# Optimization experiments

Measured on AMD Instinct MI355X. Metric: run time of the kernel, lower is better.

Reference implementation:

```python
import jax, jax.numpy as jnp
import numpy as np

B, L, PD, DIM, H, DH, DEPTH, MLP, NIMG, NCLS, TH = 2, 2048, 768, 512, 8, 64, 2, 2048, 4, 1000, 32


def _ln(x, g):
    # bias-free LayerNorm (beta buffer is zeros), eps matches torch F.layer_norm
    mu = jnp.mean(x, axis=-1, keepdims=True)
    var = jnp.var(x, axis=-1, keepdims=True)
    return (x - mu) / jnp.sqrt(var + 1e-5) * g


def _rms(x, g):
    # F.normalize(dim=-1) * sqrt(dim_head) * gamma; x: [b,h,n,dh], g: [h,1,dh]
    n = jnp.linalg.norm(x, axis=-1, keepdims=True)
    return x / jnp.maximum(n, 1e-12) * (DH ** 0.5) * g


def _attn(x, context, mask, ln_g, qg, kg, Wq, Wkv, Wo):
    b, n = x.shape[0], x.shape[1]
    xn = _ln(x, ln_g)
    kv = xn if context is None else context  # context is NOT pre-normed (matches source)
    m = kv.shape[1]
    q = (xn @ Wq).reshape(b, n, H, DH).transpose(0, 2, 1, 3)   # [b,h,n,dh]
    k, v = jnp.split(kv @ Wkv, 2, axis=-1)
    k = k.reshape(b, m, H, DH).transpose(0, 2, 1, 3)
    v = v.reshape(b, m, H, DH).transpose(0, 2, 1, 3)
    q = _rms(q, qg)
    k = _rms(k, kg)
    dots = jnp.einsum('bhid,bhjd->bhij', q, k)  # no 1/sqrt(d): QK-RMSNorm carries the scale
    neg = -jnp.finfo(dots.dtype).max
    dots = jnp.where(mask, dots, neg)
    a = jax.nn.softmax(dots, axis=-1)
    out = jnp.einsum('bhij,bhjd->bhid', a, v)
    out = out.transpose(0, 2, 1, 3).reshape(b, n, H * DH)
    return out @ Wo


def _forward(patches, ln_pe1_g, W_pe, b_pe, ln_pe2_g, pos_h_emb, pos_w_emb,
             attn_ln_g, q_g, k_g, Wq, Wkv, Wo, ff_ln_g, W1, b1, W2, b2,
             final_ln_g, pool_q, pool_ln_g, pool_q_g, pool_k_g,
             pool_Wq, pool_Wkv, pool_Wo, head_ln_g, W_head,
             pos_h, pos_w, image_ids):
    # patch embedding: LN -> Linear -> LN, then factorized 2D pos embed
    x = _ln(patches, ln_pe1_g) @ W_pe + b_pe
    x = _ln(x, ln_pe2_g)
    x = x + pos_h_emb[pos_h] + pos_w_emb[pos_w]
    # block-diagonal attention mask: tokens attend only within their image
    mask = (image_ids[:, None, :, None] == image_ids[:, None, None, :])  # [B,1,L,L]
    for i in range(DEPTH):
        x = _attn(x, None, mask, attn_ln_g[i], q_g[i], k_g[i], Wq[i], Wkv[i], Wo[i]) + x
        h = _ln(x, ff_ln_g[i]) @ W1[i] + b1[i]
        h = jax.nn.gelu(h, approximate=False)
        x = h @ W2[i] + b2[i] + x
    x = _ln(x, final_ln_g)
    # attention pooling: one learned query per packed image
    queries = jnp.broadcast_to(pool_q, (B, NIMG, DIM))
    pmask = (jnp.arange(NIMG)[None, None, :, None] == image_ids[:, None, None, :])  # [B,1,NIMG,L]
    pooled = _attn(queries, x, pmask, pool_ln_g, pool_q_g, pool_k_g, pool_Wq, pool_Wkv, pool_Wo) + queries
    return _ln(pooled, head_ln_g) @ W_head  # [B, NIMG, NCLS]


def setup_inputs() -> dict:
    key = jax.random.key(0)
    ks = jax.random.split(key, 16)
    s = 0.02
    inp = {}
    inp['patches'] = jax.random.normal(ks[0], (B, L, PD), jnp.float32)
    inp['pos_h'] = jax.random.randint(ks[1], (B, L), 0, TH)
    inp['pos_w'] = jax.random.randint(ks[2], (B, L), 0, TH)
    inp['image_ids'] = jnp.sort(jax.random.randint(ks[3], (B, L), 0, NIMG), axis=-1)
    inp['ln_pe1_g'] = jnp.ones((PD,), jnp.float32)
    inp['W_pe'] = jax.random.normal(ks[4], (PD, DIM), jnp.float32) * s
    inp['b_pe'] = jnp.zeros((DIM,), jnp.float32)
    inp['ln_pe2_g'] = jnp.ones((DIM,), jnp.float32)
    inp['pos_h_emb'] = jax.random.normal(ks[5], (TH, DIM), jnp.float32)
    inp['pos_w_emb'] = jax.random.normal(ks[6], (TH, DIM), jnp.float32)
    inp['attn_ln_g'] = jnp.ones((DEPTH, DIM), jnp.float32)
    inp['q_g'] = jnp.ones((DEPTH, H, 1, DH), jnp.float32)
    inp['k_g'] = jnp.ones((DEPTH, H, 1, DH), jnp.float32)
    inp['Wq'] = jax.random.normal(ks[7], (DEPTH, DIM, H * DH), jnp.float32) * s
    inp['Wkv'] = jax.random.normal(ks[8], (DEPTH, DIM, 2 * H * DH), jnp.float32) * s
    inp['Wo'] = jax.random.normal(ks[9], (DEPTH, H * DH, DIM), jnp.float32) * s
    inp['ff_ln_g'] = jnp.ones((DEPTH, DIM), jnp.float32)
    inp['W1'] = jax.random.normal(ks[10], (DEPTH, DIM, MLP), jnp.float32) * s
    inp['b1'] = jnp.zeros((DEPTH, MLP), jnp.float32)
    inp['W2'] = jax.random.normal(ks[11], (DEPTH, MLP, DIM), jnp.float32) * s
    inp['b2'] = jnp.zeros((DEPTH, DIM), jnp.float32)
    inp['final_ln_g'] = jnp.ones((DIM,), jnp.float32)
    inp['pool_q'] = jax.random.normal(ks[12], (DIM,), jnp.float32)
    inp['pool_ln_g'] = jnp.ones((DIM,), jnp.float32)
    inp['pool_q_g'] = jnp.ones((H, 1, DH), jnp.float32)
    inp['pool_k_g'] = jnp.ones((H, 1, DH), jnp.float32)
    inp['pool_Wq'] = jax.random.normal(ks[13], (DIM, H * DH), jnp.float32) * s
    inp['pool_Wkv'] = jax.random.normal(ks[14], (DIM, 2 * H * DH), jnp.float32) * s
    inp['pool_Wo'] = jax.random.normal(ks[15], (H * DH, DIM), jnp.float32) * s
    inp['head_ln_g'] = jnp.ones((DIM,), jnp.float32)
    inp['W_head'] = jax.random.normal(jax.random.fold_in(key, 99), (DIM, NCLS), jnp.float32) * s
    return inp


def reference(patches, pos_h, pos_w, image_ids, ln_pe1_g, W_pe, b_pe, ln_pe2_g,
              pos_h_emb, pos_w_emb, attn_ln_g, q_g, k_g, Wq, Wkv, Wo, ff_ln_g,
              W1, b1, W2, b2, final_ln_g, pool_q, pool_ln_g, pool_q_g, pool_k_g,
              pool_Wq, pool_Wkv, pool_Wo, head_ln_g, W_head):
    return _forward(patches, ln_pe1_g, W_pe, b_pe, ln_pe2_g, pos_h_emb, pos_w_emb,
                    attn_ln_g, q_g, k_g, Wq, Wkv, Wo, ff_ln_g, W1, b1, W2, b2,
                    final_ln_g, pool_q, pool_ln_g, pool_q_g, pool_k_g,
                    pool_Wq, pool_Wkv, pool_Wo, head_ln_g, W_head,
                    pos_h, pos_w, image_ids)
```

## Files before the change

### kernel.cpp

```cpp
#include <hip/hip_runtime.h>
#include <hip/hip_bf16.h>
#include <cfloat>
#include <math.h>

#define BB 2
#define LL 2048
#define PD 768
#define DIM 512
#define HH 8
#define DH 64
#define DEPTH 2
#define MLP 2048
#define NIMG 4
#define NCLS 1000
#define ROWS (BB*LL)
#define QKV (3*DIM)
#define NEGBIG (-1e30f)

typedef __hip_bfloat16 bf16;
typedef __bf16 v8bf __attribute__((ext_vector_type(8)));
typedef float f32x4 __attribute__((ext_vector_type(4)));

__device__ __forceinline__ float ldin(const void* p, size_t i, int bf) {
    return bf ? __bfloat162float(((const bf16*)p)[i]) : ((const float*)p)[i];
}
__device__ __forceinline__ float lda(const float* p, size_t i) { return p[i]; }
__device__ __forceinline__ float lda(const bf16* p, size_t i) { return __bfloat162float(p[i]); }
__device__ __forceinline__ void st(float* p, size_t i, float v) { p[i] = v; }
__device__ __forceinline__ void st(bf16* p, size_t i, float v) { p[i] = __float2bfloat16(v); }
__device__ __forceinline__ unsigned short f2bf(float x) {
    return __builtin_bit_cast(unsigned short, __float2bfloat16(x));
}
__device__ __forceinline__ float us2f(unsigned short u) {
    return __bfloat162float(__builtin_bit_cast(bf16, u));
}

__device__ __forceinline__ void stage16(const void* gsrc, void* ldst)
{
    __builtin_amdgcn_global_load_lds(
        (const __attribute__((address_space(1))) unsigned int*)(unsigned long long)gsrc,
        (__attribute__((address_space(3))) unsigned int*)(unsigned int)(unsigned long long)ldst,
        16, 0, 0);
}

__global__ void detect_dtype_kernel(const void* ones, int* flag)
{
    if (threadIdx.x == 0 && blockIdx.x == 0)
        *flag = (((const unsigned*)ones)[0] == 0x3F803F80u) ? 1 : 0;
}

__global__ void wconv_kernel(const void* __restrict__ W, int K, int N, size_t inStride,
                             bf16* __restrict__ out, size_t outOff, size_t outStride,
                             const int* dtf)
{
    __shared__ float t[32][33];
    const int bf = *dtf;
    const size_t zin = (size_t)blockIdx.z * inStride;
    const size_t zout = outOff + (size_t)blockIdx.z * outStride;
    const int kb = blockIdx.y * 32, nb = blockIdx.x * 32;
    const int tx = threadIdx.x, ty = threadIdx.y;
    #pragma unroll
    for (int u = 0; u < 4; ++u)
        t[ty + 8 * u][tx] = ldin(W, zin + (size_t)(kb + ty + 8 * u) * N + nb + tx, bf);
    __syncthreads();
    #pragma unroll
    for (int u = 0; u < 4; ++u)
        out[zout + (size_t)(nb + ty + 8 * u) * K + kb + tx] = __float2bfloat16(t[tx][ty + 8 * u]);
}

template<int RAWIN, typename TOUT>
__global__ void ln_kernel(const void* __restrict__ in, const void* __restrict__ g, size_t goff,
                          TOUT* __restrict__ out, int D, const int* dtf)
{
    __shared__ float red[16];
    const int bf = *dtf;
    const int row = blockIdx.x, tid = threadIdx.x;
    const size_t base = (size_t)row * D;
    float s = 0.f, ss = 0.f;
    for (int d = tid; d < D; d += blockDim.x) {
        float v = RAWIN ? ldin(in, base + d, bf) : ((const float*)in)[base + d];
        s += v; ss += v * v;
    }
    for (int o = 32; o; o >>= 1) { s += __shfl_xor(s, o); ss += __shfl_xor(ss, o); }
    const int wid = tid >> 6, lane = tid & 63, nw = blockDim.x >> 6;
    if (lane == 0) { red[wid] = s; red[8 + wid] = ss; }
    __syncthreads();
    if (tid == 0) {
        float a = 0.f, b = 0.f;
        for (int w = 0; w < nw; ++w) { a += red[w]; b += red[8 + w]; }
        red[0] = a; red[8] = b;
    }
    __syncthreads();
    const float mean = red[0] / D;
    const float var  = red[8] / D - mean * mean;
    const float rstd = rsqrtf(var + 1e-5f);
    for (int d = tid; d < D; d += blockDim.x) {
        float v = RAWIN ? ldin(in, base + d, bf) : ((const float*)in)[base + d];
        st(out, base + d, (v - mean) * rstd * ldin(g, goff + d, bf));
    }
}

__global__ void ln_pos_kernel(float* __restrict__ x, const void* __restrict__ g,
                              const void* __restrict__ phe, const void* __restrict__ pwe,
                              const int* __restrict__ ph, const int* __restrict__ pw,
                              const int* dtf)
{
    __shared__ float red[16];
    const int bf = *dtf;
    const int row = blockIdx.x, tid = threadIdx.x;
    const size_t base = (size_t)row * DIM;
    float s = 0.f, ss = 0.f;
    for (int d = tid; d < DIM; d += 256) { float v = x[base + d]; s += v; ss += v * v; }
    for (int o = 32; o; o >>= 1) { s += __shfl_xor(s, o); ss += __shfl_xor(ss, o); }
    const int wid = tid >> 6, lane = tid & 63;
    if (lane == 0) { red[wid] = s; red[8 + wid] = ss; }
    __syncthreads();
    if (tid == 0) {
        float a = 0.f, b = 0.f;
        for (int w = 0; w < 4; ++w) { a += red[w]; b += red[8 + w]; }
        red[0] = a; red[8] = b;
    }
    __syncthreads();
    const float mean = red[0] / DIM;
    const float var  = red[8] / DIM - mean * mean;
    const float rstd = rsqrtf(var + 1e-5f);
    const size_t hoff = (size_t)ph[row] * DIM, woff = (size_t)pw[row] * DIM;
    for (int d = tid; d < DIM; d += 256) {
        float v = (x[base + d] - mean) * rstd * ldin(g, d, bf)
                + ldin(phe, hoff + d, bf) + ldin(pwe, woff + d, bf);
        x[base + d] = v;
    }
}

#define GM 128
#define GN 64
#define GK 64

template<typename TO, int EPI>
__global__ void mgemm_kernel(const bf16* __restrict__ A, const bf16* __restrict__ Wt,
                             const void* __restrict__ bias, size_t boff,
                             const float* __restrict__ resid, TO* __restrict__ out,
                             int M, int N, int K, int kc, int gelu, const int* dtf)
{
    __shared__ __align__(16) unsigned short As[GM][GK];
    __shared__ __align__(16) unsigned short Bs[GN][GK];
    const int tid = threadIdx.x;
    const int w = tid >> 6, l = tid & 63, g = l >> 4, c = l & 15;
    const int wm = (w >> 1) * 64, wn = (w & 1) * 32;
    const int m0 = blockIdx.y * GM, n0 = blockIdx.x * GN;
    const int kbeg = blockIdx.z * kc, kend = kbeg + kc;
    const int lrow = l >> 3, lcol = (l & 7) * 8;

    f32x4 acc[4][2] = {};

    for (int k0 = kbeg; k0 < kend; k0 += GK) {
        __syncthreads();
        #pragma unroll
        for (int u = 0; u < 4; ++u) {
            const int rr = 32 * w + 8 * u;
            stage16(A + (size_t)(m0 + rr + lrow) * K + k0 + lcol, &As[rr][0]);
        }
        #pragma unroll
        for (int u = 0; u < 2; ++u) {
            const int rr = 16 * w + 8 * u;
            stage16(Wt + (size_t)(n0 + rr + lrow) * K + k0 + lcol, &Bs[rr][0]);
        }
        __syncthreads();
        #pragma unroll
        for (int kk = 0; kk < GK; kk += 32) {
            v8bf av[4], bv[2];
            #pragma unroll
            for (int i = 0; i < 4; ++i) av[i] = *(const v8bf*)&As[wm + i * 16 + c][kk + 8 * g];
            #pragma unroll
            for (int j = 0; j < 2; ++j) bv[j] = *(const v8bf*)&Bs[wn + j * 16 + c][kk + 8 * g];
            #pragma unroll
            for (int i = 0; i < 4; ++i)
                #pragma unroll
                for (int j = 0; j < 2; ++j)
                    acc[i][j] = __builtin_amdgcn_mfma_f32_16x16x32_bf16(av[i], bv[j], acc[i][j], 0, 0, 0);
        }
    }

    if (EPI == 0) {
        float* po = (float*)out + (size_t)blockIdx.z * M * N;
        #pragma unroll
        for (int i = 0; i < 4; ++i) {
            const int rb = m0 + wm + i * 16 + 4 * g;
            #pragma unroll
            for (int j = 0; j < 2; ++j) {
                const int col = n0 + wn + j * 16 + c;
                #pragma unroll
                for (int r = 0; r < 4; ++r)
                    po[(size_t)(rb + r) * N + col] = acc[i][j][r];
            }
        }
    } else {
        const int bf = *dtf;
        #pragma unroll
        for (int i = 0; i < 4; ++i) {
            const int rb = m0 + wm + i * 16 + 4 * g;
            #pragma unroll
            for (int j = 0; j < 2; ++j) {
                const int col = n0 + wn + j * 16 + c;
                const float bvl = bias ? ldin(bias, boff + col, bf) : 0.f;
                #pragma unroll
                for (int r = 0; r < 4; ++r) {
                    float v = acc[i][j][r] + bvl;
                    if (gelu) v = 0.5f * v * (1.f + erff(v * 0.70710678118654752f));
                    if (resid) v += resid[(size_t)(rb + r) * N + col];
                    st(out, (size_t)(rb + r) * N + col, v);
                }
            }
        }
    }
}

template<typename TO>
__global__ void mcomb_kernel(const float* __restrict__ part, int S, const void* __restrict__ bias,
                             size_t boff, const float* __restrict__ resid, TO* __restrict__ out,
                             size_t MN, int N, int gelu, const int* dtf)
{
    const size_t idx = (size_t)blockIdx.x * 256 + threadIdx.x;
    if (idx >= MN) return;
    float v = 0.f;
    for (int s = 0; s < S; ++s) v += part[(size_t)s * MN + idx];
    const int bf = *dtf;
    if (bias) v += ldin(bias, boff + (int)(idx % N), bf);
    if (gelu) v = 0.5f * v * (1.f + erff(v * 0.70710678118654752f));
    if (resid) v += resid[idx];
    st(out, idx, v);
}

__global__ void comb_ln_kernel(const float* __restrict__ part, int S,
                               const void* __restrict__ bias, size_t boff,
                               float* __restrict__ x, const void* __restrict__ g, size_t goff,
                               bf16* __restrict__ xb, const int* dtf)
{
    __shared__ float red[16];
    const int bf = *dtf;
    const int row = blockIdx.x, tid = threadIdx.x;
    const size_t base = (size_t)row * DIM;
    float v[2];
    float s = 0.f, ss = 0.f;
    #pragma unroll
    for (int u = 0; u < 2; ++u) {
        const int d = tid + 256 * u;
        float a = 0.f;
        for (int sc = 0; sc < S; ++sc) a += part[(size_t)sc * ROWS * DIM + base + d];
        if (bias) a += ldin(bias, boff + d, bf);
        a += x[base + d];
        x[base + d] = a;
        v[u] = a; s += a; ss += a * a;
    }
    for (int o = 32; o; o >>= 1) { s += __shfl_xor(s, o); ss += __shfl_xor(ss, o); }
    const int wid = tid >> 6, lane = tid & 63;
    if (lane == 0) { red[wid] = s; red[8 + wid] = ss; }
    __syncthreads();
    if (tid == 0) {
        float a = 0.f, b = 0.f;
        for (int w2 = 0; w2 < 4; ++w2) { a += red[w2]; b += red[8 + w2]; }
        red[0] = a; red[8] = b;
    }
    __syncthreads();
    const float mean = red[0] / DIM;
    const float var  = red[8] / DIM - mean * mean;
    const float rstd = rsqrtf(var + 1e-5f);
    #pragma unroll
    for (int u = 0; u < 2; ++u) {
        const int d = tid + 256 * u;
        xb[base + d] = __float2bfloat16((v[u] - mean) * rstd * ldin(g, goff + d, bf));
    }
}

#define TS 16
template<typename TA, typename TO>
__global__ void gemm_kernel(const TA* __restrict__ A, const void* __restrict__ W, size_t woff,
                            const void* __restrict__ bias, size_t boff,
                            const float* __restrict__ resid, TO* __restrict__ out,
                            int M, int N, int K, int gelu, const int* dtf)
{
    __shared__ float As[TS][TS + 1];
    __shared__ float Bs[TS][TS + 1];
    const int bf = *dtf;
    const int tx = threadIdx.x, ty = threadIdx.y;
    const int col = blockIdx.x * TS + tx;
    const int row = blockIdx.y * TS + ty;
    float acc = 0.f;
    for (int k0 = 0; k0 < K; k0 += TS) {
        const int ka = k0 + tx;
        As[ty][tx] = (row < M && ka < K) ? lda(A, (size_t)row * K + ka) : 0.f;
        const int kb = k0 + ty;
        Bs[ty][tx] = (col < N && kb < K) ? ldin(W, woff + (size_t)kb * N + col, bf) : 0.f;
        __syncthreads();
        #pragma unroll
        for (int kk = 0; kk < TS; ++kk) acc = fmaf(As[ty][kk], Bs[kk][tx], acc);
        __syncthreads();
    }
    if (row < M && col < N) {
        if (bias) acc += ldin(bias, boff + col, bf);
        if (gelu) acc = 0.5f * acc * (1.f + erff(acc * 0.70710678118654752f));
        if (resid) acc += resid[(size_t)row * N + col];
        st(out, (size_t)row * N + col, acc);
    }
}

__global__ void rms_kernel(float* __restrict__ buf, const void* __restrict__ g, size_t goff,
                           int stride, int colbase, const int* dtf)
{
    const int bf = *dtf;
    const int r = blockIdx.x, h = blockIdx.y, lane = threadIdx.x;
    float* p = buf + (size_t)r * stride + colbase + h * DH;
    const float v = p[lane];
    float ss = v * v;
    for (int o = 32; o; o >>= 1) ss += __shfl_xor(ss, o);
    const float norm = sqrtf(ss);
    const float sc = 8.0f / fmaxf(norm, 1e-12f);
    p[lane] = v * sc * ldin(g, goff + h * DH + lane, bf);
}

__global__ void rms2_kernel(bf16* __restrict__ buf, int stride,
                            const void* __restrict__ g0, size_t g0off,
                            int base1, const void* __restrict__ g1, size_t g1off,
                            int nslot, const int* dtf)
{
    const int bf = *dtf;
    const int tid = threadIdx.x;
    const int s = tid >> 4, li = tid & 15;
    if (s >= nslot) return;
    const int h = s & 7;
    const int colbase = (s < 8) ? 0 : base1;
    const void* g = (s < 8) ? g0 : g1;
    const size_t go = ((s < 8) ? g0off : g1off) + h * DH + li * 4;
    bf16* p = buf + (size_t)blockIdx.x * stride + colbase + h * DH + li * 4;
    ushort4 v = *(const ushort4*)p;
    const float f0 = us2f(v.x), f1 = us2f(v.y), f2 = us2f(v.z), f3 = us2f(v.w);
    float ss = f0 * f0 + f1 * f1 + f2 * f2 + f3 * f3;
    ss += __shfl_xor(ss, 8); ss += __shfl_xor(ss, 4);
    ss += __shfl_xor(ss, 2); ss += __shfl_xor(ss, 1);
    const float sc = 8.0f / fmaxf(sqrtf(ss), 1e-12f);
    ushort4 o;
    o.x = f2bf(f0 * sc * ldin(g, go + 0, bf));
    o.y = f2bf(f1 * sc * ldin(g, go + 1, bf));
    o.z = f2bf(f2 * sc * ldin(g, go + 2, bf));
    o.w = f2bf(f3 * sc * ldin(g, go + 3, bf));
    *(ushort4*)p = o;
}

#define QT 64
#define KT 64
#define LP 72

__global__ void flash_attn_kernel(const bf16* __restrict__ q, int qstr,
                                  const bf16* __restrict__ kpt, const bf16* __restrict__ vpt,
                                  int kvstr, const int* __restrict__ ids,
                                  bf16* __restrict__ out)
{
    __shared__ __align__(16) unsigned short Qs[QT][LP];
    __shared__ __align__(16) unsigned short Ks[KT][LP];
    __shared__ __align__(16) unsigned short Vt[DH][LP];
    __shared__ __align__(16) unsigned short Ps[QT][LP];
    __shared__ __align__(16) int ids_s[KT];
    __shared__ __align__(16) int qids_s[QT];
    __shared__ int range_s[2];

    const int tid = threadIdx.x;
    const int bid = blockIdx.x;
    const int s0 = (bid & 7) * 64 + (bid >> 3);
    const int qb = (s0 & 31) * QT;
    const int h = (s0 >> 5) & 7;
    const int b = s0 >> 8;
    const int w = tid >> 6, l = tid & 63, g = l >> 4, c = l & 15;

    {
        const int r = tid >> 2, c0 = (tid & 3) << 4;
        const bf16* qp = q + (size_t)(b * LL + qb + r) * qstr + h * DH + c0;
        *(int4*)&Qs[r][c0]     = *(const int4*)qp;
        *(int4*)&Qs[r][c0 + 8] = *(const int4*)(qp + 8);
        if (tid < QT) qids_s[tid] = ids[b * LL + qb + tid];
    }
    if (tid == 0) {
        const int* bp = ids + b * LL;
        const int qlo = bp[qb], qhi = bp[qb + QT - 1];
        int lo = 0, hi = LL;
        while (lo < hi) { int mid = (lo + hi) >> 1; if (bp[mid] < qlo) lo = mid + 1; else hi = mid; }
        range_s[0] = lo;
        int lo2 = 0, hi2 = LL;
        while (lo2 < hi2) { int mid = (lo2 + hi2) >> 1; if (bp[mid] <= qhi) lo2 = mid + 1; else hi2 = mid; }
        range_s[1] = lo2;
    }
    __syncthreads();

    const int myid = qids_s[16 * w + c];
    const v8bf qf0 = *(const v8bf*)&Qs[16 * w + c][8 * g];
    const v8bf qf1 = *(const v8bf*)&Qs[16 * w + c][8 * g + 32];
    const int kb_start = (range_s[0] / KT) * KT;
    const int kb_end = range_s[1];

    f32x4 o[4];
    #pragma unroll
    for (int dt = 0; dt < 4; ++dt) o[dt] = (f32x4){0.f, 0.f, 0.f, 0.f};
    float mr = NEGBIG, lr = 0.f;

    for (int kb = kb_start; kb < kb_end; kb += KT) {
        __syncthreads();
        {
            const int r = tid >> 2, c0 = (tid & 3) << 4;
            const bf16* kp = kpt + (size_t)(b * LL + kb + r) * kvstr + h * DH + c0;
            *(int4*)&Ks[r][c0]     = *(const int4*)kp;
            *(int4*)&Ks[r][c0 + 8] = *(const int4*)(kp + 8);
        }
        {
            const int kp2 = (tid & 31) * 2, db = (tid >> 5) * 8;
            const bf16* v0p = vpt + (size_t)(b * LL + kb + kp2) * kvstr + h * DH + db;
            const bf16* v1p = v0p + kvstr;
            const ushort4 a0 = *(const ushort4*)v0p;
            const ushort4 a1 = *(const ushort4*)(v0p + 4);
            const ushort4 b0 = *(const ushort4*)v1p;
            const ushort4 b1 = *(const ushort4*)(v1p + 4);
            const unsigned short* ap0 = (const unsigned short*)&a0;
            const unsigned short* ap1 = (const unsigned short*)&a1;
            const unsigned short* bp0 = (const unsigned short*)&b0;
            const unsigned short* bp1 = (const unsigned short*)&b1;
            #pragma unroll
            for (int j = 0; j < 4; ++j) {
                *(unsigned int*)&Vt[db + j][kp2]     = (unsigned)ap0[j] | ((unsigned)bp0[j] << 16);
                *(unsigned int*)&Vt[db + 4 + j][kp2] = (unsigned)ap1[j] | ((unsigned)bp1[j] << 16);
            }
        }
        if (tid < KT) ids_s[tid] = ids[b * LL + kb + tid];
        __syncthreads();

        f32x4 stt[4];
        #pragma unroll
        for (int t = 0; t < 4; ++t) {
            stt[t] = (f32x4){0.f, 0.f, 0.f, 0.f};
            v8bf kf0 = *(const v8bf*)&Ks[16 * t + c][8 * g];
            v8bf kf1 = *(const v8bf*)&Ks[16 * t + c][8 * g + 32];
            stt[t] = __builtin_amdgcn_mfma_f32_16x16x32_bf16(kf0, qf0, stt[t], 0, 0, 0);
            stt[t] = __builtin_amdgcn_mfma_f32_16x16x32_bf16(kf1, qf1, stt[t], 0, 0, 0);
        }

        float sv[16]; int mk[16];
        float tmax = NEGBIG;
        #pragma unroll
        for (int t = 0; t < 4; ++t) {
            int4 iv = *(const int4*)&ids_s[16 * t + 4 * g];
            const int* ivp = (const int*)&iv;
            #pragma unroll
            for (int r = 0; r < 4; ++r) {
                float s = stt[t][r];
                int m = (ivp[r] == myid);
                sv[4 * t + r] = s; mk[4 * t + r] = m;
                if (m) tmax = fmaxf(tmax, s);
            }
        }
        tmax = fmaxf(tmax, __shfl_xor(tmax, 16));
        tmax = fmaxf(tmax, __shfl_xor(tmax, 32));
        const float mnew = fmaxf(mr, tmax);
        const float al = __expf(mr - mnew);
        float tsum = 0.f;
        #pragma unroll
        for (int t = 0; t < 4; ++t) {
            ushort4 pk;
            unsigned short* pp = (unsigned short*)&pk;
            #pragma unroll
            for (int r = 0; r < 4; ++r) {
                float p = mk[4 * t + r] ? __expf(sv[4 * t + r] - mnew) : 0.f;
                tsum += p;
                pp[r] = f2bf(p);
            }
            *(ushort4*)&Ps[16 * w + c][16 * t + 4 * g] = pk;
        }
        tsum += __shfl_xor(tsum, 16);
        tsum += __shfl_xor(tsum, 32);
        lr = lr * al + tsum;
        mr = mnew;

        const float a0 = __shfl(al, 4 * g + 0);
        const float a1 = __shfl(al, 4 * g + 1);
        const float a2 = __shfl(al, 4 * g + 2);
        const float a3 = __shfl(al, 4 * g + 3);
        #pragma unroll
        for (int dt = 0; dt < 4; ++dt) {
            o[dt][0] *= a0; o[dt][1] *= a1; o[dt][2] *= a2; o[dt][3] *= a3;
        }

        const v8bf pf0 = *(const v8bf*)&Ps[16 * w + c][8 * g];
        const v8bf pf1 = *(const v8bf*)&Ps[16 * w + c][8 * g + 32];
        #pragma unroll
        for (int dt = 0; dt < 4; ++dt) {
            v8bf vf0 = *(const v8bf*)&Vt[16 * dt + c][8 * g];
            v8bf vf1 = *(const v8bf*)&Vt[16 * dt + c][8 * g + 32];
            o[dt] = __builtin_amdgcn_mfma_f32_16x16x32_bf16(pf0, vf0, o[dt], 0, 0, 0);
            o[dt] = __builtin_amdgcn_mfma_f32_16x16x32_bf16(pf1, vf1, o[dt], 0, 0, 0);
        }
    }

    const float li0 = 1.f / __shfl(lr, 4 * g + 0);
    const float li1 = 1.f / __shfl(lr, 4 * g + 1);
    const float li2 = 1.f / __shfl(lr, 4 * g + 2);
    const float li3 = 1.f / __shfl(lr, 4 * g + 3);
    #pragma unroll
    for (int dt = 0; dt < 4; ++dt) {
        bf16* op = out + (size_t)(b * LL + qb + 16 * w) * DIM + h * DH + 16 * dt + c;
        op[(size_t)(4 * g + 0) * DIM] = __float2bfloat16(o[dt][0] * li0);
        op[(size_t)(4 * g + 1) * DIM] = __float2bfloat16(o[dt][1] * li1);
        op[(size_t)(4 * g + 2) * DIM] = __float2bfloat16(o[dt][2] * li2);
        op[(size_t)(4 * g + 3) * DIM] = __float2bfloat16(o[dt][3] * li3);
    }
}

#define PCH 16
#define PCK (LL / PCH)

__global__ void pool_attn_part_kernel(const float* __restrict__ q, const bf16* __restrict__ kv,
                                      int kvs, const int* __restrict__ ids,
                                      float* __restrict__ ppm, float* __restrict__ ppl,
                                      float* __restrict__ ppo)
{
    const int iq = blockIdx.x & (NIMG - 1), ch = blockIdx.x >> 2;
    const int h = blockIdx.y, b = blockIdx.z;
    const int tid = threadIdx.x;
    const int qrow = b * NIMG + iq;
    const int j0 = ch * PCK;
    __shared__ float qs[DH];
    __shared__ float s[PCK];

    qs[tid] = q[(size_t)qrow * DIM + h * DH + tid];
    __syncthreads();
    #pragma unroll
    for (int u = 0; u < 2; ++u) {
        const int j = j0 + tid + 64 * u;
        const bf16* kp = kv + (size_t)(b * LL + j) * kvs + h * DH;
        float d = 0.f;
        #pragma unroll
        for (int t = 0; t < DH; t += 8) {
            int4 kvv = *(const int4*)&kp[t];
            const unsigned short* uu = (const unsigned short*)&kvv;
            #pragma unroll
            for (int z = 0; z < 8; ++z) d = fmaf(qs[t + z], us2f(uu[z]), d);
        }
        s[tid + 64 * u] = (ids[b * LL + j] == iq) ? d : NEGBIG;
    }
    __syncthreads();
    float m = fmaxf(s[tid], s[tid + 64]);
    for (int o = 32; o; o >>= 1) m = fmaxf(m, __shfl_xor(m, o));
    const float p0 = __expf(s[tid] - m), p1 = __expf(s[tid + 64] - m);
    float ls = p0 + p1;
    for (int o = 32; o; o >>= 1) ls += __shfl_xor(ls, o);
    s[tid] = p0; s[tid + 64] = p1;
    __syncthreads();
    float acc = 0.f;
    for (int jj = 0; jj < PCK; ++jj)
        acc += s[jj] * __bfloat162float(kv[(size_t)(b * LL + j0 + jj) * kvs + DIM + h * DH + tid]);
    const int p = ((b * HH + h) * NIMG + iq) * PCH + ch;
    if (tid == 0) { ppm[p] = m; ppl[p] = ls; }
    ppo[(size_t)p * DH + tid] = acc;
}

__global__ void pool_attn_comb_kernel(const float* __restrict__ ppm, const float* __restrict__ ppl,
                                      const float* __restrict__ ppo, float* __restrict__ out)
{
    const int iq = blockIdx.x, h = blockIdx.y, b = blockIdx.z;
    const int d = threadIdx.x;
    const int pb = ((b * HH + h) * NIMG + iq) * PCH;
    float mstar = NEGBIG;
    #pragma unroll
    for (int ch = 0; ch < PCH; ++ch) mstar = fmaxf(mstar, ppm[pb + ch]);
    float lsum = 0.f, osum = 0.f;
    #pragma unroll
    for (int ch = 0; ch < PCH; ++ch) {
        const float w = __expf(ppm[pb + ch] - mstar);
        lsum += ppl[pb + ch] * w;
        osum += ppo[(size_t)(pb + ch) * DH + d] * w;
    }
    out[(size_t)(b * NIMG + iq) * DIM + h * DH + d] = osum / lsum;
}

__global__ void fill_q_kernel(float* __restrict__ queries, const void* __restrict__ pool_q,
                              const int* dtf)
{
    const int bf = *dtf;
    const int idx = blockIdx.x * blockDim.x + threadIdx.x;
    if (idx < BB * NIMG * DIM) queries[idx] = ldin(pool_q, idx % DIM, bf);
}

__global__ void write_out_kernel(const float* __restrict__ in, void* __restrict__ out, int n,
                                 const int* dtf)
{
    const int bf = *dtf;
    const int idx = blockIdx.x * blockDim.x + threadIdx.x;
    if (idx < n) {
        if (bf) ((bf16*)out)[idx] = __float2bfloat16(in[idx]);
        else    ((float*)out)[idx] = in[idx];
    }
}

extern "C" void kernel_launch(void* const* d_in, const int* in_sizes, int n_in,
                              void* d_out, int out_size, void* d_ws, size_t ws_size,
                              hipStream_t stream)
{
    const void* patches   = d_in[0];
    const int*  pos_h     = (const int*) d_in[1];
    const int*  pos_w     = (const int*) d_in[2];
    const int*  image_ids = (const int*) d_in[3];
    const void* ln_pe1_g  = d_in[4];
    const void* W_pe      = d_in[5];
    const void* b_pe      = d_in[6];
    const void* ln_pe2_g  = d_in[7];
    const void* pos_h_emb = d_in[8];
    const void* pos_w_emb = d_in[9];
    const void* attn_ln_g = d_in[10];
    const void* q_g       = d_in[11];
    const void* k_g       = d_in[12];
    const void* Wq        = d_in[13];
    const void* Wkv       = d_in[14];
    const void* Wo        = d_in[15];
    const void* ff_ln_g   = d_in[16];
    const void* W1        = d_in[17];
    const void* b1        = d_in[18];
    const void* W2        = d_in[19];
    const void* b2        = d_in[20];
    const void* final_ln_g= d_in[21];
    const void* pool_q    = d_in[22];
    const void* pool_ln_g = d_in[23];
    const void* pool_q_g  = d_in[24];
    const void* pool_k_g  = d_in[25];
    const void* pool_Wq   = d_in[26];
    const void* pool_Wkv  = d_in[27];
    const void* pool_Wo   = d_in[28];
    const void* head_ln_g = d_in[29];
    const void* W_head    = d_in[30];

    char* p = (char*)d_ws;
    int* flag = (int*)p;                         p += 256;
    float* x   = (float*)p;                      p += (size_t)ROWS * DIM * 4;
    bf16* xb   = (bf16*)p;                       p += (size_t)ROWS * PD * 2;
    bf16* qkvb = (bf16*)p;  bf16* hb = qkvb;     p += (size_t)ROWS * MLP * 2;
    bf16* wpeT  = (bf16*)p;                      p += (size_t)DIM * PD * 2;
    bf16* wqkvT = (bf16*)p;                      p += (size_t)DEPTH * QKV * DIM * 2;
    bf16* woT   = (bf16*)p;                      p += (size_t)DEPTH * DIM * DIM * 2;
    bf16* w1T   = (bf16*)p;                      p += (size_t)DEPTH * MLP * DIM * 2;
    bf16* w2T   = (bf16*)p;                      p += (size_t)DEPTH * DIM * MLP * 2;
    bf16* pkvT  = (bf16*)p;                      p += (size_t)2 * DIM * DIM * 2;
    float* queries = (float*)p;                  p += 4096 * 4;
    float* qp      = (float*)p;                  p += 4096 * 4;
    float* pattn   = (float*)p;                  p += 4096 * 4;
    float* pooled  = (float*)p;                  p += 4096 * 4;
    bf16*  pln     = (bf16*)p;                   p += 4096 * 2;
    float* hout    = (float*)p;                  p += 8192 * 4;
    float* ppm     = (float*)p;                  p += 1024 * 4;
    float* ppl     = (float*)p;                  p += 1024 * 4;
    float* ppo     = (float*)p;                  p += (size_t)1024 * DH * 4;
    float* part    = (float*)p;                  p += (size_t)4 * ROWS * DIM * 4;

    const dim3 blk256(256);
    const dim3 blkG(TS, TS);
    const dim3 blkT(32, 8);

    detect_dtype_kernel<<<1, 1, 0, stream>>>(ln_pe1_g, flag);

    wconv_kernel<<<dim3(DIM / 32, PD / 32, 1), blkT, 0, stream>>>(
        W_pe, PD, DIM, 0, wpeT, 0, 0, flag);
    wconv_kernel<<<dim3(DIM / 32, DIM / 32, DEPTH), blkT, 0, stream>>>(
        Wq, DIM, DIM, (size_t)DIM * DIM, wqkvT, 0, (size_t)QKV * DIM, flag);
    wconv_kernel<<<dim3(2 * DIM / 32, DIM / 32, DEPTH), blkT, 0, stream>>>(
        Wkv, DIM, 2 * DIM, (size_t)DIM * 2 * DIM, wqkvT, (size_t)DIM * DIM, (size_t)QKV * DIM, flag);
    wconv_kernel<<<dim3(DIM / 32, DIM / 32, DEPTH), blkT, 0, stream>>>(
        Wo, DIM, DIM, (size_t)DIM * DIM, woT, 0, (size_t)DIM * DIM, flag);
    wconv_kernel<<<dim3(MLP / 32, DIM / 32, DEPTH), blkT, 0, stream>>>(
        W1, DIM, MLP, (size_t)DIM * MLP, w1T, 0, (size_t)MLP * DIM, flag);
    wconv_kernel<<<dim3(DIM / 32, MLP / 32, DEPTH), blkT, 0, stream>>>(
        W2, MLP, DIM, (size_t)MLP * DIM, w2T, 0, (size_t)DIM * MLP, flag);
    wconv_kernel<<<dim3(2 * DIM / 32, DIM / 32, 1), blkT, 0, stream>>>(
        pool_Wkv, DIM, 2 * DIM, 0, pkvT, 0, 0, flag);

    ln_kernel<1, bf16><<<ROWS, blk256, 0, stream>>>(patches, ln_pe1_g, 0, xb, PD, flag);
    mgemm_kernel<float, 0><<<dim3(DIM / GN, ROWS / GM, 2), blk256, 0, stream>>>(
        xb, wpeT, nullptr, 0, nullptr, part, ROWS, DIM, PD, PD / 2, 0, flag);
    mcomb_kernel<float><<<(ROWS * DIM + 255) / 256, blk256, 0, stream>>>(
        part, 2, b_pe, 0, nullptr, x, (size_t)ROWS * DIM, DIM, 0, flag);
    ln_pos_kernel<<<ROWS, blk256, 0, stream>>>(x, ln_pe2_g, pos_h_emb, pos_w_emb, pos_h, pos_w, flag);
    ln_kernel<0, bf16><<<ROWS, blk256, 0, stream>>>(x, attn_ln_g, 0, xb, DIM, flag);

    for (int i = 0; i < DEPTH; ++i) {
        mgemm_kernel<bf16, 1><<<dim3(QKV / GN, ROWS / GM, 1), blk256, 0, stream>>>(
            xb, wqkvT + (size_t)i * QKV * DIM, nullptr, 0, nullptr, qkvb,
            ROWS, QKV, DIM, DIM, 0, flag);
        rms2_kernel<<<ROWS, blk256, 0, stream>>>(
            qkvb, QKV, q_g, (size_t)i * HH * DH, DIM, k_g, (size_t)i * HH * DH, 16, flag);
        flash_attn_kernel<<<dim3(512), blk256, 0, stream>>>(
            qkvb, QKV, qkvb + DIM, qkvb + 2 * DIM, QKV, image_ids, xb);
        mgemm_kernel<float, 0><<<dim3(DIM / GN, ROWS / GM, 2), blk256, 0, stream>>>(
            xb, woT + (size_t)i * DIM * DIM, nullptr, 0, nullptr, part,
            ROWS, DIM, DIM, DIM / 2, 0, flag);
        comb_ln_kernel<<<ROWS, blk256, 0, stream>>>(
            part, 2, nullptr, 0, x, ff_ln_g, (size_t)i * DIM, xb, flag);
        mgemm_kernel<bf16, 1><<<dim3(MLP / GN, ROWS / GM, 1), blk256, 0, stream>>>(
            xb, w1T + (size_t)i * MLP * DIM, b1, (size_t)i * MLP, nullptr, hb,
            ROWS, MLP, DIM, DIM, 1, flag);
        mgemm_kernel<float, 0><<<dim3(DIM / GN, ROWS / GM, 4), blk256, 0, stream>>>(
            hb, w2T + (size_t)i * DIM * MLP, nullptr, 0, nullptr, part,
            ROWS, DIM, MLP, MLP / 4, 0, flag);
        const void* gnext = (i + 1 < DEPTH) ? attn_ln_g : final_ln_g;
        const size_t gnoff = (i + 1 < DEPTH) ? (size_t)(i + 1) * DIM : 0;
        comb_ln_kernel<<<ROWS, blk256, 0, stream>>>(
            part, 4, b2, (size_t)i * DIM, x, gnext, gnoff, xb, flag);
    }

    fill_q_kernel<<<(BB * NIMG * DIM + 255) / 256, blk256, 0, stream>>>(queries, pool_q, flag);
    ln_kernel<0, bf16><<<BB * NIMG, blk256, 0, stream>>>(queries, pool_ln_g, 0, pln, DIM, flag);
    gemm_kernel<bf16, float><<<dim3(DIM / TS, 1), blkG, 0, stream>>>(
        pln, pool_Wq, 0, nullptr, 0, nullptr, qp, BB * NIMG, DIM, DIM, 0, flag);
    mgemm_kernel<bf16, 1><<<dim3(2 * DIM / GN, ROWS / GM, 1), blk256, 0, stream>>>(
        xb, pkvT, nullptr, 0, nullptr, qkvb, ROWS, 2 * DIM, DIM, DIM, 0, flag);
    rms_kernel<<<dim3(BB * NIMG, HH), dim3(64), 0, stream>>>(
        qp, pool_q_g, 0, DIM, 0, flag);
    rms2_kernel<<<ROWS, blk256, 0, stream>>>(
        qkvb, 2 * DIM, pool_k_g, 0, 0, nullptr, 0, 8, flag);
    pool_attn_part_kernel<<<dim3(NIMG * PCH, HH, BB), dim3(64), 0, stream>>>(
        qp, qkvb, 2 * DIM, image_ids, ppm, ppl, ppo);
    pool_attn_comb_kernel<<<dim3(NIMG, HH, BB), dim3(64), 0, stream>>>(ppm, ppl, ppo, pattn);
    gemm_kernel<float, float><<<dim3(DIM / TS, 1), blkG, 0, stream>>>(
        pattn, pool_Wo, 0, nullptr, 0, queries, pooled, BB * NIMG, DIM, DIM, 0, flag);

    ln_kernel<0, bf16><<<BB * NIMG, blk256, 0, stream>>>(pooled, head_ln_g, 0, pln, DIM, flag);
    gemm_kernel<bf16, float><<<dim3((NCLS + TS - 1) / TS, 1), blkG, 0, stream>>>(
        pln, W_head, 0, nullptr, 0, nullptr, hout, BB * NIMG, NCLS, DIM, 0, flag);
    write_out_kernel<<<(BB * NIMG * NCLS + 255) / 256, blk256, 0, stream>>>(
        hout, d_out, BB * NIMG * NCLS, flag);
}
```

Before: 473.4 us.

## Fuse patch-embed combine, LN and pos-embed; stream K from global in attention

Measured after the change: 495.4 us. 4.7% more time.

```diff
diff --git a/kernel.cpp b/kernel.cpp
--- a/kernel.cpp
+++ b/kernel.cpp
@@ -100,35 +100,69 @@
     }
 }
 
-__global__ void ln_pos_kernel(float* __restrict__ x, const void* __restrict__ g,
-                              const void* __restrict__ phe, const void* __restrict__ pwe,
-                              const int* __restrict__ ph, const int* __restrict__ pw,
-                              const int* dtf)
+__global__ void patch_fuse_kernel(const float* __restrict__ part,
+                                  const void* __restrict__ b_pe,
+                                  const void* __restrict__ g1,
+                                  const void* __restrict__ phe, const void* __restrict__ pwe,
+                                  const int* __restrict__ ph, const int* __restrict__ pw,
+                                  const void* __restrict__ g2,
+                                  float* __restrict__ x, bf16* __restrict__ xb,
+                                  const int* dtf)
 {
     __shared__ float red[16];
     const int bf = *dtf;
     const int row = blockIdx.x, tid = threadIdx.x;
     const size_t base = (size_t)row * DIM;
+    const int wid = tid >> 6, lane = tid & 63;
+    float v[2];
     float s = 0.f, ss = 0.f;
-    for (int d = tid; d < DIM; d += 256) { float v = x[base + d]; s += v; ss += v * v; }
+    #pragma unroll
+    for (int u = 0; u < 2; ++u) {
+        const int d = tid + 256 * u;
+        float a = part[base + d] + part[(size_t)ROWS * DIM + base + d] + ldin(b_pe, d, bf);
+        v[u] = a; s += a; ss += a * a;
+    }
     for (int o = 32; o; o >>= 1) { s += __shfl_xor(s, o); ss += __shfl_xor(ss, o); }
-    const int wid = tid >> 6, lane = tid & 63;
     if (lane == 0) { red[wid] = s; red[8 + wid] = ss; }
     __syncthreads();
     if (tid == 0) {
         float a = 0.f, b = 0.f;
-        for (int w = 0; w < 4; ++w) { a += red[w]; b += red[8 + w]; }
+        for (int w2 = 0; w2 < 4; ++w2) { a += red[w2]; b += red[8 + w2]; }
+        red[0] = a; red[8] = b;
+    }
+    __syncthreads();
+    {
+        const float mean = red[0] / DIM;
+        const float var  = red[8] / DIM - mean * mean;
+        const float rstd = rsqrtf(var + 1e-5f);
+        const size_t hoff = (size_t)ph[row] * DIM, woff = (size_t)pw[row] * DIM;
+        s = 0.f; ss = 0.f;
+        #pragma unroll
+        for (int u = 0; u < 2; ++u) {
+            const int d = tid + 256 * u;
+            float a = (v[u] - mean) * rstd * ldin(g1, d, bf)
+                    + ldin(phe, hoff + d, bf) + ldin(pwe, woff + d, bf);
+            x[base + d] = a;
+            v[u] = a; s += a; ss += a * a;
+        }
+    }
+    for (int o = 32; o; o >>= 1) { s += __shfl_xor(s, o); ss += __shfl_xor(ss, o); }
+    __syncthreads();
+    if (lane == 0) { red[wid] = s; red[8 + wid] = ss; }
+    __syncthreads();
+    if (tid == 0) {
+        float a = 0.f, b = 0.f;
+        for (int w2 = 0; w2 < 4; ++w2) { a += red[w2]; b += red[8 + w2]; }
         red[0] = a; red[8] = b;
     }
     __syncthreads();
     const float mean = red[0] / DIM;
     const float var  = red[8] / DIM - mean * mean;
     const float rstd = rsqrtf(var + 1e-5f);
-    const size_t hoff = (size_t)ph[row] * DIM, woff = (size_t)pw[row] * DIM;
-    for (int d = tid; d < DIM; d += 256) {
-        float v = (x[base + d] - mean) * rstd * ldin(g, d, bf)
-                + ldin(phe, hoff + d, bf) + ldin(pwe, woff + d, bf);
-        x[base + d] = v;
+    #pragma unroll
+    for (int u = 0; u < 2; ++u) {
+        const int d = tid + 256 * u;
+        xb[base + d] = __float2bfloat16((v[u] - mean) * rstd * ldin(g2, d, bf));
     }
 }
 
@@ -213,22 +247,6 @@
             }
         }
     }
-}
-
-template<typename TO>
-__global__ void mcomb_kernel(const float* __restrict__ part, int S, const void* __restrict__ bias,
-                             size_t boff, const float* __restrict__ resid, TO* __restrict__ out,
-                             size_t MN, int N, int gelu, const int* dtf)
-{
-    const size_t idx = (size_t)blockIdx.x * 256 + threadIdx.x;
-    if (idx >= MN) return;
-    float v = 0.f;
-    for (int s = 0; s < S; ++s) v += part[(size_t)s * MN + idx];
-    const int bf = *dtf;
-    if (bias) v += ldin(bias, boff + (int)(idx % N), bf);
-    if (gelu) v = 0.5f * v * (1.f + erff(v * 0.70710678118654752f));
-    if (resid) v += resid[idx];
-    st(out, idx, v);
 }
 
 __global__ void comb_ln_kernel(const float* __restrict__ part, int S,
@@ -356,7 +374,6 @@
                                   bf16* __restrict__ out)
 {
     __shared__ __align__(16) unsigned short Qs[QT][LP];
-    __shared__ __align__(16) unsigned short Ks[KT][LP];
     __shared__ __align__(16) unsigned short Vt[DH][LP];
     __shared__ __align__(16) unsigned short Ps[QT][LP];
     __shared__ __align__(16) int ids_s[KT];
@@ -401,41 +418,50 @@
     for (int dt = 0; dt < 4; ++dt) o[dt] = (f32x4){0.f, 0.f, 0.f, 0.f};
     float mr = NEGBIG, lr = 0.f;
 
+    const int kp2 = (tid & 31) * 2, db = (tid >> 5) * 8;
+    ushort4 va0, va1, vb0, vb1;
+    int idv = 0;
+    {
+        const bf16* v0p = vpt + (size_t)(b * LL + kb_start + kp2) * kvstr + h * DH + db;
+        const bf16* v1p = v0p + kvstr;
+        va0 = *(const ushort4*)v0p; va1 = *(const ushort4*)(v0p + 4);
+        vb0 = *(const ushort4*)v1p; vb1 = *(const ushort4*)(v1p + 4);
+        if (tid < KT) idv = ids[b * LL + kb_start + tid];
+    }
+
     for (int kb = kb_start; kb < kb_end; kb += KT) {
         __syncthreads();
         {
-            const int r = tid >> 2, c0 = (tid & 3) << 4;
-            const bf16* kp = kpt + (size_t)(b * LL + kb + r) * kvstr + h * DH + c0;
-            *(int4*)&Ks[r][c0]     = *(const int4*)kp;
-            *(int4*)&Ks[r][c0 + 8] = *(const int4*)(kp + 8);
-        }
-        {
-            const int kp2 = (tid & 31) * 2, db = (tid >> 5) * 8;
-            const bf16* v0p = vpt + (size_t)(b * LL + kb + kp2) * kvstr + h * DH + db;
-            const bf16* v1p = v0p + kvstr;
-            const ushort4 a0 = *(const ushort4*)v0p;
-            const ushort4 a1 = *(const ushort4*)(v0p + 4);
-            const ushort4 b0 = *(const ushort4*)v1p;
-            const ushort4 b1 = *(const ushort4*)(v1p + 4);
-            const unsigned short* ap0 = (const unsigned short*)&a0;
-            const unsigned short* ap1 = (const unsigned short*)&a1;
-            const unsigned short* bp0 = (const unsigned short*)&b0;
-            const unsigned short* bp1 = (const unsigned short*)&b1;
+            const unsigned short* ap0 = (const unsigned short*)&va0;
+            const unsigned short* ap1 = (const unsigned short*)&va1;
+            const unsigned short* bp0 = (const unsigned short*)&vb0;
+            const unsigned short* bp1 = (const unsigned short*)&vb1;
             #pragma unroll
             for (int j = 0; j < 4; ++j) {
                 *(unsigned int*)&Vt[db + j][kp2]     = (unsigned)ap0[j] | ((unsigned)bp0[j] << 16);
                 *(unsigned int*)&Vt[db + 4 + j][kp2] = (unsigned)ap1[j] | ((unsigned)bp1[j] << 16);
             }
-        }
-        if (tid < KT) ids_s[tid] = ids[b * LL + kb + tid];
-        __syncthreads();
-
+            if (tid < KT) ids_s[tid] = idv;
+        }
+        if (kb + KT < kb_end) {
+            const bf16* v0p = vpt + (size_t)(b * LL + kb + KT + kp2) * kvstr + h * DH + db;
+            const bf16* v1p = v0p + kvstr;
+            va0 = *(const ushort4*)v0p; va1 = *(const ushort4*)(v0p + 4);
+            vb0 = *(const ushort4*)v1p; vb1 = *(const ushort4*)(v1p + 4);
+            if (tid < KT) idv = ids[b * LL + kb + KT + tid];
+        }
+        asm volatile("s_waitcnt lgkmcnt(0)" ::: "memory");
+        __builtin_amdgcn_s_barrier();
+        __builtin_amdgcn_sched_barrier(0);
+
+        const bf16* kbase = kpt + (size_t)(b * LL + kb) * kvstr + h * DH;
         f32x4 stt[4];
         #pragma unroll
         for (int t = 0; t < 4; ++t) {
+            const bf16* kp = kbase + (size_t)(16 * t + c) * kvstr + 8 * g;
+            v8bf kf0 = *(const v8bf*)kp;
+            v8bf kf1 = *(const v8bf*)(kp + 32);
             stt[t] = (f32x4){0.f, 0.f, 0.f, 0.f};
-            v8bf kf0 = *(const v8bf*)&Ks[16 * t + c][8 * g];
-            v8bf kf1 = *(const v8bf*)&Ks[16 * t + c][8 * g + 32];
             stt[t] = __builtin_amdgcn_mfma_f32_16x16x32_bf16(kf0, qf0, stt[t], 0, 0, 0);
             stt[t] = __builtin_amdgcn_mfma_f32_16x16x32_bf16(kf1, qf1, stt[t], 0, 0, 0);
         }
@@ -678,10 +704,8 @@
     ln_kernel<1, bf16><<<ROWS, blk256, 0, stream>>>(patches, ln_pe1_g, 0, xb, PD, flag);
     mgemm_kernel<float, 0><<<dim3(DIM / GN, ROWS / GM, 2), blk256, 0, stream>>>(
         xb, wpeT, nullptr, 0, nullptr, part, ROWS, DIM, PD, PD / 2, 0, flag);
-    mcomb_kernel<float><<<(ROWS * DIM + 255) / 256, blk256, 0, stream>>>(
-        part, 2, b_pe, 0, nullptr, x, (size_t)ROWS * DIM, DIM, 0, flag);
-    ln_pos_kernel<<<ROWS, blk256, 0, stream>>>(x, ln_pe2_g, pos_h_emb, pos_w_emb, pos_h, pos_w, flag);
-    ln_kernel<0, bf16><<<ROWS, blk256, 0, stream>>>(x, attn_ln_g, 0, xb, DIM, flag);
+    patch_fuse_kernel<<<ROWS, blk256, 0, stream>>>(
+        part, b_pe, ln_pe2_g, pos_h_emb, pos_w_emb, pos_h, pos_w, attn_ln_g, x, xb, flag);
 
     for (int i = 0; i < DEPTH; ++i) {
         mgemm_kernel<bf16, 1><<<dim3(QKV / GN, ROWS / GM, 1), blk256, 0, stream>>>(
```
